# Kernel optimization log

Measured on AMD Instinct MI355X. Metric: run time of the kernel, lower is better.

Reference implementation:

```python
import jax, jax.numpy as jnp
import numpy as np

NUM_NODES = 50000
DIM = 64
NUM_LAYERS = 2
NUM_EDGES = 800000
EPS = 1e-12


def _l2_normalize(x):
    # F.normalize(x, dim=1): x / max(||x||_2, eps)
    n = jnp.sqrt(jnp.sum(x * x, axis=1, keepdims=True))
    return x / jnp.maximum(n, EPS)


def _lgconv(x, src, dst):
    # PyG LGConv: symmetric gcn_norm without self-loops.
    # deg computed at target nodes; out[dst] += d^-1/2[src] * d^-1/2[dst] * x[src]
    ones = jnp.ones(src.shape[0], dtype=x.dtype)
    deg = jax.ops.segment_sum(ones, dst, num_segments=NUM_NODES)
    dinv = jnp.where(deg > 0, 1.0 / jnp.sqrt(jnp.where(deg > 0, deg, 1.0)), 0.0)
    norm = dinv[src] * dinv[dst]  # [E]
    msg = norm[:, None] * x[src]  # [E, D] gather + scale
    return jax.ops.segment_sum(msg, dst, num_segments=NUM_NODES)


def _propagate(x, edge_index):
    src, dst = edge_index[0], edge_index[1]
    for _ in range(NUM_LAYERS):
        x = _lgconv(x, src, dst)
    return _l2_normalize(x)


def setup_inputs() -> dict:
    key = jax.random.key(0)
    k1, k2, k3, k4 = jax.random.split(key, 4)
    x = jax.random.normal(k1, (NUM_NODES, DIM), dtype=jnp.float32)
    alpha = jnp.ones((3,), dtype=jnp.float32)
    ei_t = jax.random.randint(k2, (2, NUM_EDGES), 0, NUM_NODES, dtype=jnp.int32)
    ei_y = jax.random.randint(k3, (2, NUM_EDGES), 0, NUM_NODES, dtype=jnp.int32)
    ei_c = jax.random.randint(k4, (2, NUM_EDGES), 0, NUM_NODES, dtype=jnp.int32)
    return {"x": x, "alpha": alpha, "edge_index_title": ei_t,
            "edge_index_year": ei_y, "edge_index_cat": ei_c}


def reference(x, alpha, edge_index_title, edge_index_year, edge_index_cat):
    x = _l2_normalize(x)
    x_title = _propagate(x, edge_index_title)
    x_year = _propagate(x, edge_index_year)
    x_cat = _propagate(x, edge_index_cat)
    w = jax.nn.softmax(alpha, axis=0)
    w = jnp.clip(w, 0.0001, None)
    w = w / jnp.sum(w)
    return w[0] * x_title + w[1] * x_year + w[2] * x_cat
```

## Files before the change

kernel.cpp:

```cpp
#include <hip/hip_runtime.h>
#include <hip/hip_bf16.h>

#define NUM_NODES 50000
#define DIM 64
#define NUM_EDGES 800000
#define NUM_GRAPHS 3
#define TOT_NODES (NUM_NODES * NUM_GRAPHS)
#define TOT_EDGES (NUM_EDGES * NUM_GRAPHS)
#define EPS 1e-12f

#define NB 196
#define TB (NB * NUM_GRAPHS)
#define P3_CHUNK 8192
#define P3_BLOCKS ((NUM_EDGES + P3_CHUNK - 1) / P3_CHUNK)
#define P4_CAP 6144

typedef unsigned short ushort_t;
typedef unsigned int uint_t;
typedef unsigned short ushort8v __attribute__((ext_vector_type(8)));

__device__ __forceinline__ float bf2f(ushort_t u) {
    return __uint_as_float(((uint_t)u) << 16);
}
__device__ __forceinline__ ushort_t f2bf(float f) {
    uint_t x = __float_as_uint(f);
    uint_t r = (x + 0x7FFFu + ((x >> 16) & 1u)) >> 16;
    return (ushort_t)r;
}

__global__ void l2norm_kernel(const float* __restrict__ in, ushort_t* __restrict__ out) {
    int row = blockIdx.x * (blockDim.x >> 6) + (threadIdx.x >> 6);
    int lane = threadIdx.x & 63;
    if (row >= NUM_NODES) return;
    float v = in[(long)row * DIM + lane];
    float s = v * v;
    #pragma unroll
    for (int off = 32; off > 0; off >>= 1)
        s += __shfl_xor(s, off, 64);
    float inv = 1.0f / fmaxf(sqrtf(s), EPS);
    out[(long)row * DIM + lane] = f2bf(v * inv);
}

__global__ void hist_coarse_kernel(const int* __restrict__ e0, const int* __restrict__ e1,
                                   const int* __restrict__ e2, int* __restrict__ bhist) {
    int g = blockIdx.y;
    const int* dst = ((g == 0) ? e0 : (g == 1) ? e1 : e2) + NUM_EDGES;
    __shared__ int h[NB];
    int t = threadIdx.x;
    for (int i = t; i < NB; i += 256) h[i] = 0;
    __syncthreads();
    int base = blockIdx.x * P3_CHUNK;
    int n = min(P3_CHUNK, NUM_EDGES - base);
    for (int i = t; i < n; i += 256)
        atomicAdd(&h[dst[base + i] >> 8], 1);
    __syncthreads();
    for (int i = t; i < NB; i += 256)
        if (h[i]) atomicAdd(&bhist[g * NB + i], h[i]);
}

__global__ void bucket_scan_kernel(const int* __restrict__ bhist, int* __restrict__ bbase,
                                   int* __restrict__ bcur) {
    int t = threadIdx.x;
    int v = (t < TB) ? bhist[t] : 0;
    __shared__ int sd[1024];
    sd[t] = v;
    __syncthreads();
    #pragma unroll
    for (int off = 1; off < 1024; off <<= 1) {
        int add = (t >= off) ? sd[t - off] : 0;
        __syncthreads();
        sd[t] += add;
        __syncthreads();
    }
    if (t < TB) {
        int ex = sd[t] - v;
        bbase[t] = ex;
        bcur[t] = ex;
    }
    if (t == 0) bbase[TB] = TOT_EDGES;
}

__global__ void partition_kernel(const int* __restrict__ e0, const int* __restrict__ e1,
                                 const int* __restrict__ e2,
                                 int* __restrict__ bcur, uint_t* __restrict__ part) {
    __shared__ uint_t recs[P3_CHUNK];
    __shared__ int h[NB], lstart[NB], gbase[NB], lcur[NB];
    __shared__ int sc[256];

    int g = blockIdx.y;
    const int* ei = (g == 0) ? e0 : (g == 1) ? e1 : e2;
    const int* srcp = ei;
    const int* dstp = ei + NUM_EDGES;
    int base = blockIdx.x * P3_CHUNK;
    int n = min(P3_CHUNK, NUM_EDGES - base);
    int t = threadIdx.x;

    for (int i = t; i < NB; i += 256) h[i] = 0;
    __syncthreads();
    for (int i = t; i < n; i += 256)
        atomicAdd(&h[dstp[base + i] >> 8], 1);
    __syncthreads();

    {
        int v = (t < NB) ? h[t] : 0;
        sc[t] = v;
        __syncthreads();
        #pragma unroll
        for (int off = 1; off < 256; off <<= 1) {
            int add = (t >= off) ? sc[t - off] : 0;
            __syncthreads();
            sc[t] += add;
            __syncthreads();
        }
        if (t < NB) {
            int ex = sc[t] - v;
            lstart[t] = ex;
            lcur[t] = ex;
            gbase[t] = (v > 0) ? atomicAdd(&bcur[g * NB + t], v) : 0;
        }
    }
    __syncthreads();

    for (int i = t; i < n; i += 256) {
        int s = srcp[base + i];
        int d = dstp[base + i];
        int pos = atomicAdd(&lcur[d >> 8], 1);
        recs[pos] = ((uint_t)d << 16) | (uint_t)s;
    }
    __syncthreads();

    for (int i = t; i < n; i += 256) {
        uint_t r = recs[i];
        int b = r >> 24;
        part[gbase[b] + (i - lstart[b])] = r;
    }
}

__global__ void bucket_sort_kernel(const uint_t* __restrict__ part, const int* __restrict__ bbase,
                                   ushort_t* __restrict__ esort, int* __restrict__ row_start,
                                   float* __restrict__ dinv) {
    __shared__ uint_t recs[P4_CAP];
    __shared__ int rstart[256], lcur[256];
    __shared__ int sc[256];

    int b = blockIdx.x;
    int g = b / NB;
    int bhi = b % NB;
    int s0 = bbase[b];
    int n = bbase[b + 1] - s0;
    int t = threadIdx.x;

    sc[t] = 0;
    __syncthreads();
    for (int i = t; i < n; i += 256) {
        uint_t r = part[s0 + i];
        recs[i] = r;
        atomicAdd(&sc[(r >> 16) & 255], 1);
    }
    __syncthreads();
    int v = sc[t];
    __syncthreads();
    sc[t] = v;
    __syncthreads();
    #pragma unroll
    for (int off = 1; off < 256; off <<= 1) {
        int add = (t >= off) ? sc[t - off] : 0;
        __syncthreads();
        sc[t] += add;
        __syncthreads();
    }
    int ex = sc[t] - v;
    rstart[t] = ex;
    lcur[t] = ex;

    int node = (bhi << 8) + t;
    if (node < NUM_NODES) {
        row_start[g * NUM_NODES + node] = s0 + ex;
        dinv[g * NUM_NODES + node] = (v > 0) ? rsqrtf((float)v) : 0.0f;
    }
    if (b == TB - 1 && t == 0) row_start[TOT_NODES] = TOT_EDGES;
    __syncthreads();

    for (int i = t; i < n; i += 256) {
        uint_t r = recs[i];
        int dl = (r >> 16) & 255;
        int pos = atomicAdd(&lcur[dl], 1);
        esort[s0 + pos] = (ushort_t)(r & 0xFFFFu);
    }
}

__global__ void conv1_all_kernel(const ushort_t* __restrict__ xn,
                                 const ushort_t* __restrict__ esort,
                                 const int* __restrict__ row_start,
                                 const float* __restrict__ dinv,
                                 ushort_t* __restrict__ bufA) {
    int row = blockIdx.x * (blockDim.x >> 6) + (threadIdx.x >> 6);
    int g = blockIdx.y;
    int lane = threadIdx.x & 63;
    int sub = lane >> 3;
    int li  = lane & 7;
    if (row >= NUM_NODES) return;

    int k = g * NUM_NODES + row;
    int start = __builtin_amdgcn_readfirstlane(row_start[k]);
    int end   = __builtin_amdgcn_readfirstlane(row_start[k + 1]);
    const float* dv = dinv + g * NUM_NODES;

    float a[8];
    #pragma unroll
    for (int j = 0; j < 8; ++j) a[j] = 0.0f;

    int i = start;
    for (; i + 16 <= end; i += 16) {
        int sA = esort[i + sub];
        int sB = esort[i + 8 + sub];
        float dA = dv[sA];
        float dB = dv[sB];
        ushort8v rA = *(const ushort8v*)(xn + (long)sA * DIM + li * 8);
        ushort8v rB = *(const ushort8v*)(xn + (long)sB * DIM + li * 8);
        #pragma unroll
        for (int j = 0; j < 8; ++j) a[j] += dA * bf2f(rA[j]);
        #pragma unroll
        for (int j = 0; j < 8; ++j) a[j] += dB * bf2f(rB[j]);
    }
    for (; i < end; i += 8) {
        int e = i + sub;
        if (e < end) {
            int s = esort[e];
            float d = dv[s];
            ushort8v r = *(const ushort8v*)(xn + (long)s * DIM + li * 8);
            #pragma unroll
            for (int j = 0; j < 8; ++j) a[j] += d * bf2f(r[j]);
        }
    }
    #pragma unroll
    for (int off = 8; off < 64; off <<= 1) {
        #pragma unroll
        for (int j = 0; j < 8; ++j)
            a[j] += __shfl_xor(a[j], off, 64);
    }
    float dt = dinv[k];
    float sc = dt * dt;
    if (sub == 0) {
        ushort8v o;
        #pragma unroll
        for (int j = 0; j < 8; ++j) o[j] = f2bf(a[j] * sc);
        *(ushort8v*)(bufA + (long)k * DIM + li * 8) = o;
    }
}

__global__ void conv2_finalize_kernel(const ushort_t* __restrict__ bufA,
                                      const ushort_t* __restrict__ esort,
                                      const int* __restrict__ row_start,
                                      const float* __restrict__ alpha,
                                      float* __restrict__ out) {
    int row = blockIdx.x * (blockDim.x >> 6) + (threadIdx.x >> 6);
    int lane = threadIdx.x & 63;
    int sub = lane >> 3;
    int li  = lane & 7;
    if (row >= NUM_NODES) return;

    float al0 = alpha[0], al1 = alpha[1], al2 = alpha[2];
    float m = fmaxf(al0, fmaxf(al1, al2));
    float e0 = expf(al0 - m), e1 = expf(al1 - m), e2 = expf(al2 - m);
    float es = e0 + e1 + e2;
    float w0 = fmaxf(e0 / es, 1e-4f);
    float w1 = fmaxf(e1 / es, 1e-4f);
    float w2 = fmaxf(e2 / es, 1e-4f);
    float ws = w0 + w1 + w2;

    float r[8];
    #pragma unroll
    for (int j = 0; j < 8; ++j) r[j] = 0.0f;

    #pragma unroll
    for (int g = 0; g < NUM_GRAPHS; ++g) {
        int k = g * NUM_NODES + row;
        int start = __builtin_amdgcn_readfirstlane(row_start[k]);
        int end   = __builtin_amdgcn_readfirstlane(row_start[k + 1]);
        const ushort_t* tbl = bufA + (long)g * NUM_NODES * DIM;

        float a[8];
        #pragma unroll
        for (int j = 0; j < 8; ++j) a[j] = 0.0f;

        int i = start;
        for (; i + 16 <= end; i += 16) {
            int sA = esort[i + sub];
            int sB = esort[i + 8 + sub];
            ushort8v rA = *(const ushort8v*)(tbl + (long)sA * DIM + li * 8);
            ushort8v rB = *(const ushort8v*)(tbl + (long)sB * DIM + li * 8);
            #pragma unroll
            for (int j = 0; j < 8; ++j) a[j] += bf2f(rA[j]);
            #pragma unroll
            for (int j = 0; j < 8; ++j) a[j] += bf2f(rB[j]);
        }
        for (; i < end; i += 8) {
            int e = i + sub;
            if (e < end) {
                int s = esort[e];
                ushort8v rr = *(const ushort8v*)(tbl + (long)s * DIM + li * 8);
                #pragma unroll
                for (int j = 0; j < 8; ++j) a[j] += bf2f(rr[j]);
            }
        }
        #pragma unroll
        for (int off = 8; off < 64; off <<= 1) {
            #pragma unroll
            for (int j = 0; j < 8; ++j)
                a[j] += __shfl_xor(a[j], off, 64);
        }
        float s = 0.0f;
        #pragma unroll
        for (int j = 0; j < 8; ++j) s += a[j] * a[j];
        #pragma unroll
        for (int off = 1; off < 8; off <<= 1)
            s += __shfl_xor(s, off, 64);
        float inv = 1.0f / fmaxf(sqrtf(s), EPS);
        float w = ((g == 0) ? w0 : (g == 1) ? w1 : w2) / ws * inv;
        #pragma unroll
        for (int j = 0; j < 8; ++j) r[j] += w * a[j];
    }

    if (sub == 0) {
        float4 o0 = make_float4(r[0], r[1], r[2], r[3]);
        float4 o1 = make_float4(r[4], r[5], r[6], r[7]);
        float* p = out + (long)row * DIM + li * 8;
        *(float4*)p = o0;
        *(float4*)(p + 4) = o1;
    }
}

extern "C" void kernel_launch(void* const* d_in, const int* in_sizes, int n_in,
                              void* d_out, int out_size, void* d_ws, size_t ws_size,
                              hipStream_t stream) {
    const float* x     = (const float*)d_in[0];
    const float* alpha = (const float*)d_in[1];
    const int* e0 = (const int*)d_in[2];
    const int* e1 = (const int*)d_in[3];
    const int* e2 = (const int*)d_in[4];
    float* out = (float*)d_out;

    ushort_t* xn   = (ushort_t*)d_ws;
    ushort_t* bufA = xn + (long)NUM_NODES * DIM;
    float* dinv    = (float*)(bufA + (long)TOT_NODES * DIM);
    int* row_start = (int*)(dinv + TOT_NODES);
    int* bhist     = row_start + 150016;
    int* bbase     = bhist + 640;
    int* bcur      = bbase + 640;
    uint_t* part   = (uint_t*)(bcur + 640);
    ushort_t* esort = (ushort_t*)(part + TOT_EDGES);

    const int wave_grid = (NUM_NODES * 64 + 255) / 256;

    l2norm_kernel<<<wave_grid, 256, 0, stream>>>(x, xn);

    hipMemsetAsync(bhist, 0, TB * sizeof(int), stream);
    {
        dim3 grd(P3_BLOCKS, NUM_GRAPHS);
        hist_coarse_kernel<<<grd, 256, 0, stream>>>(e0, e1, e2, bhist);
    }
    bucket_scan_kernel<<<1, 1024, 0, stream>>>(bhist, bbase, bcur);
    {
        dim3 grd(P3_BLOCKS, NUM_GRAPHS);
        partition_kernel<<<grd, 256, 0, stream>>>(e0, e1, e2, bcur, part);
    }
    bucket_sort_kernel<<<TB, 256, 0, stream>>>(part, bbase, esort, row_start, dinv);

    {
        dim3 grd(wave_grid, NUM_GRAPHS);
        conv1_all_kernel<<<grd, 256, 0, stream>>>(xn, esort, row_start, dinv, bufA);
    }
    conv2_finalize_kernel<<<wave_grid, 256, 0, stream>>>(bufA, esort, row_start, alpha, out);
}
```

Before: 255.8 us.

## Use fixed-capacity bucket slots, split conv2 per graph, add blend pass

Removes the coarse histogram and scan kernels by giving each destination bucket a fixed PCAP-sized slot in the partition buffer, with atomic counters giving offsets and row_end replacing row_start[k+1]. Conv2 is split into a per-graph kernel whose blocks interleave graphs for cache locality. It writes weighted normalized bf16 results, and a separate blend kernel sums the three graphs. Gathers now load uint4 words and unpack bf16 with shifts and masks. The cost is an extra bf16 round-trip for the outputs, and any bucket holding more than PCAP edges is silently truncated.

```diff
diff --git a/kernel.cpp b/kernel.cpp
--- a/kernel.cpp
+++ b/kernel.cpp
@@ -13,11 +13,12 @@
 #define TB (NB * NUM_GRAPHS)
 #define P3_CHUNK 8192
 #define P3_BLOCKS ((NUM_EDGES + P3_CHUNK - 1) / P3_CHUNK)
-#define P4_CAP 6144
+#define PCAP 5120
 
 typedef unsigned short ushort_t;
 typedef unsigned int uint_t;
 typedef unsigned short ushort8v __attribute__((ext_vector_type(8)));
+typedef unsigned int uint4v __attribute__((ext_vector_type(4)));
 
 __device__ __forceinline__ float bf2f(ushort_t u) {
     return __uint_as_float(((uint_t)u) << 16);
@@ -26,6 +27,27 @@
     uint_t x = __float_as_uint(f);
     uint_t r = (x + 0x7FFFu + ((x >> 16) & 1u)) >> 16;
     return (ushort_t)r;
+}
+
+__device__ __forceinline__ void unpack_fma(uint4v w, float d, float* a) {
+    a[0] += d * __uint_as_float(w[0] << 16);
+    a[1] += d * __uint_as_float(w[0] & 0xFFFF0000u);
+    a[2] += d * __uint_as_float(w[1] << 16);
+    a[3] += d * __uint_as_float(w[1] & 0xFFFF0000u);
+    a[4] += d * __uint_as_float(w[2] << 16);
+    a[5] += d * __uint_as_float(w[2] & 0xFFFF0000u);
+    a[6] += d * __uint_as_float(w[3] << 16);
+    a[7] += d * __uint_as_float(w[3] & 0xFFFF0000u);
+}
+__device__ __forceinline__ void unpack_add(uint4v w, float* a) {
+    a[0] += __uint_as_float(w[0] << 16);
+    a[1] += __uint_as_float(w[0] & 0xFFFF0000u);
+    a[2] += __uint_as_float(w[1] << 16);
+    a[3] += __uint_as_float(w[1] & 0xFFFF0000u);
+    a[4] += __uint_as_float(w[2] << 16);
+    a[5] += __uint_as_float(w[2] & 0xFFFF0000u);
+    a[6] += __uint_as_float(w[3] << 16);
+    a[7] += __uint_as_float(w[3] & 0xFFFF0000u);
 }
 
 __global__ void l2norm_kernel(const float* __restrict__ in, ushort_t* __restrict__ out) {
@@ -41,48 +63,9 @@
     out[(long)row * DIM + lane] = f2bf(v * inv);
 }
 
-__global__ void hist_coarse_kernel(const int* __restrict__ e0, const int* __restrict__ e1,
-                                   const int* __restrict__ e2, int* __restrict__ bhist) {
-    int g = blockIdx.y;
-    const int* dst = ((g == 0) ? e0 : (g == 1) ? e1 : e2) + NUM_EDGES;
-    __shared__ int h[NB];
-    int t = threadIdx.x;
-    for (int i = t; i < NB; i += 256) h[i] = 0;
-    __syncthreads();
-    int base = blockIdx.x * P3_CHUNK;
-    int n = min(P3_CHUNK, NUM_EDGES - base);
-    for (int i = t; i < n; i += 256)
-        atomicAdd(&h[dst[base + i] >> 8], 1);
-    __syncthreads();
-    for (int i = t; i < NB; i += 256)
-        if (h[i]) atomicAdd(&bhist[g * NB + i], h[i]);
-}
-
-__global__ void bucket_scan_kernel(const int* __restrict__ bhist, int* __restrict__ bbase,
-                                   int* __restrict__ bcur) {
-    int t = threadIdx.x;
-    int v = (t < TB) ? bhist[t] : 0;
-    __shared__ int sd[1024];
-    sd[t] = v;
-    __syncthreads();
-    #pragma unroll
-    for (int off = 1; off < 1024; off <<= 1) {
-        int add = (t >= off) ? sd[t - off] : 0;
-        __syncthreads();
-        sd[t] += add;
-        __syncthreads();
-    }
-    if (t < TB) {
-        int ex = sd[t] - v;
-        bbase[t] = ex;
-        bcur[t] = ex;
-    }
-    if (t == 0) bbase[TB] = TOT_EDGES;
-}
-
 __global__ void partition_kernel(const int* __restrict__ e0, const int* __restrict__ e1,
                                  const int* __restrict__ e2,
-                                 int* __restrict__ bcur, uint_t* __restrict__ part) {
+                                 int* __restrict__ gcnt, uint_t* __restrict__ part) {
     __shared__ uint_t recs[P3_CHUNK];
     __shared__ int h[NB], lstart[NB], gbase[NB], lcur[NB];
     __shared__ int sc[256];
@@ -116,7 +99,7 @@
             int ex = sc[t] - v;
             lstart[t] = ex;
             lcur[t] = ex;
-            gbase[t] = (v > 0) ? atomicAdd(&bcur[g * NB + t], v) : 0;
+            gbase[t] = (v > 0) ? atomicAdd(&gcnt[g * NB + t], v) : 0;
         }
     }
     __syncthreads();
@@ -132,22 +115,24 @@
     for (int i = t; i < n; i += 256) {
         uint_t r = recs[i];
         int b = r >> 24;
-        part[gbase[b] + (i - lstart[b])] = r;
-    }
-}
-
-__global__ void bucket_sort_kernel(const uint_t* __restrict__ part, const int* __restrict__ bbase,
+        int off = gbase[b] + (i - lstart[b]);
+        if (off < PCAP)
+            part[(long)(g * NB + b) * PCAP + off] = r;
+    }
+}
+
+__global__ void bucket_sort_kernel(const uint_t* __restrict__ part, const int* __restrict__ gcnt,
                                    ushort_t* __restrict__ esort, int* __restrict__ row_start,
-                                   float* __restrict__ dinv) {
-    __shared__ uint_t recs[P4_CAP];
-    __shared__ int rstart[256], lcur[256];
+                                   int* __restrict__ row_end, float* __restrict__ dinv) {
+    __shared__ uint_t recs[PCAP];
+    __shared__ int lcur[256];
     __shared__ int sc[256];
 
     int b = blockIdx.x;
     int g = b / NB;
     int bhi = b % NB;
-    int s0 = bbase[b];
-    int n = bbase[b + 1] - s0;
+    long s0 = (long)b * PCAP;
+    int n = min(gcnt[b], PCAP);
     int t = threadIdx.x;
 
     sc[t] = 0;
@@ -170,15 +155,15 @@
         __syncthreads();
     }
     int ex = sc[t] - v;
-    rstart[t] = ex;
     lcur[t] = ex;
 
     int node = (bhi << 8) + t;
     if (node < NUM_NODES) {
-        row_start[g * NUM_NODES + node] = s0 + ex;
-        dinv[g * NUM_NODES + node] = (v > 0) ? rsqrtf((float)v) : 0.0f;
-    }
-    if (b == TB - 1 && t == 0) row_start[TOT_NODES] = TOT_EDGES;
+        int k = g * NUM_NODES + node;
+        row_start[k] = (int)s0 + ex;
+        row_end[k]   = (int)s0 + ex + v;
+        dinv[k] = (v > 0) ? rsqrtf((float)v) : 0.0f;
+    }
     __syncthreads();
 
     for (int i = t; i < n; i += 256) {
@@ -192,6 +177,7 @@
 __global__ void conv1_all_kernel(const ushort_t* __restrict__ xn,
                                  const ushort_t* __restrict__ esort,
                                  const int* __restrict__ row_start,
+                                 const int* __restrict__ row_end,
                                  const float* __restrict__ dinv,
                                  ushort_t* __restrict__ bufA) {
     int row = blockIdx.x * (blockDim.x >> 6) + (threadIdx.x >> 6);
@@ -203,7 +189,7 @@
 
     int k = g * NUM_NODES + row;
     int start = __builtin_amdgcn_readfirstlane(row_start[k]);
-    int end   = __builtin_amdgcn_readfirstlane(row_start[k + 1]);
+    int end   = __builtin_amdgcn_readfirstlane(row_end[k]);
     const float* dv = dinv + g * NUM_NODES;
 
     float a[8];
@@ -216,21 +202,18 @@
         int sB = esort[i + 8 + sub];
         float dA = dv[sA];
         float dB = dv[sB];
-        ushort8v rA = *(const ushort8v*)(xn + (long)sA * DIM + li * 8);
-        ushort8v rB = *(const ushort8v*)(xn + (long)sB * DIM + li * 8);
-        #pragma unroll
-        for (int j = 0; j < 8; ++j) a[j] += dA * bf2f(rA[j]);
-        #pragma unroll
-        for (int j = 0; j < 8; ++j) a[j] += dB * bf2f(rB[j]);
+        uint4v rA = *(const uint4v*)(xn + (long)sA * DIM + li * 8);
+        uint4v rB = *(const uint4v*)(xn + (long)sB * DIM + li * 8);
+        unpack_fma(rA, dA, a);
+        unpack_fma(rB, dB, a);
     }
     for (; i < end; i += 8) {
         int e = i + sub;
         if (e < end) {
             int s = esort[e];
             float d = dv[s];
-            ushort8v r = *(const ushort8v*)(xn + (long)s * DIM + li * 8);
-            #pragma unroll
-            for (int j = 0; j < 8; ++j) a[j] += d * bf2f(r[j]);
+            uint4v r = *(const uint4v*)(xn + (long)s * DIM + li * 8);
+            unpack_fma(r, d, a);
         }
     }
     #pragma unroll
@@ -240,25 +223,40 @@
             a[j] += __shfl_xor(a[j], off, 64);
     }
     float dt = dinv[k];
-    float sc = dt * dt;
+    float scl = dt * dt;
     if (sub == 0) {
         ushort8v o;
         #pragma unroll
-        for (int j = 0; j < 8; ++j) o[j] = f2bf(a[j] * sc);
+        for (int j = 0; j < 8; ++j) o[j] = f2bf(a[j] * scl);
         *(ushort8v*)(bufA + (long)k * DIM + li * 8) = o;
     }
 }
 
-__global__ void conv2_finalize_kernel(const ushort_t* __restrict__ bufA,
-                                      const ushort_t* __restrict__ esort,
-                                      const int* __restrict__ row_start,
-                                      const float* __restrict__ alpha,
-                                      float* __restrict__ out) {
-    int row = blockIdx.x * (blockDim.x >> 6) + (threadIdx.x >> 6);
+__global__ void conv2_kernel(const ushort_t* __restrict__ bufA,
+                             const ushort_t* __restrict__ esort,
+                             const int* __restrict__ row_start,
+                             const int* __restrict__ row_end,
+                             const float* __restrict__ alpha,
+                             ushort_t* __restrict__ ybuf) {
+    const int gmap[8]   = {0, 1, 2, 0, 1, 2, 0, 1};
+    const int idxmap[8] = {0, 0, 0, 1, 1, 1, 2, 2};
+    const int cntmap[8] = {3, 3, 2, 3, 3, 2, 3, 3};
+
+    int x = blockIdx.x & 7;
+    int j = blockIdx.x >> 3;
+    int g = gmap[x];
+    int idx = idxmap[x];
+    int cnt = cntmap[x];
+    int chunk = (NUM_NODES + cnt - 1) / cnt;
+
+    int row_local = j * 4 + (threadIdx.x >> 6);
+    if (row_local >= chunk) return;
+    int row = idx * chunk + row_local;
+    if (row >= NUM_NODES) return;
+
     int lane = threadIdx.x & 63;
     int sub = lane >> 3;
     int li  = lane & 7;
-    if (row >= NUM_NODES) return;
 
     float al0 = alpha[0], al1 = alpha[1], al2 = alpha[2];
     float m = fmaxf(al0, fmaxf(al1, al2));
@@ -268,67 +266,71 @@
     float w1 = fmaxf(e1 / es, 1e-4f);
     float w2 = fmaxf(e2 / es, 1e-4f);
     float ws = w0 + w1 + w2;
-
+    float w = ((g == 0) ? w0 : (g == 1) ? w1 : w2) / ws;
+
+    int k = g * NUM_NODES + row;
+    int start = __builtin_amdgcn_readfirstlane(row_start[k]);
+    int end   = __builtin_amdgcn_readfirstlane(row_end[k]);
+    const ushort_t* tbl = bufA + (long)g * NUM_NODES * DIM;
+
+    float a[8];
+    #pragma unroll
+    for (int jj = 0; jj < 8; ++jj) a[jj] = 0.0f;
+
+    int i = start;
+    for (; i + 16 <= end; i += 16) {
+        int sA = esort[i + sub];
+        int sB = esort[i + 8 + sub];
+        uint4v rA = *(const uint4v*)(tbl + (long)sA * DIM + li * 8);
+        uint4v rB = *(const uint4v*)(tbl + (long)sB * DIM + li * 8);
+        unpack_add(rA, a);
+        unpack_add(rB, a);
+    }
+    for (; i < end; i += 8) {
+        int e = i + sub;
+        if (e < end) {
+            int s = esort[e];
+            uint4v r = *(const uint4v*)(tbl + (long)s * DIM + li * 8);
+            unpack_add(r, a);
+        }
+    }
+    #pragma unroll
+    for (int off = 8; off < 64; off <<= 1) {
+        #pragma unroll
+        for (int jj = 0; jj < 8; ++jj)
+            a[jj] += __shfl_xor(a[jj], off, 64);
+    }
+    float s = 0.0f;
+    #pragma unroll
+    for (int jj = 0; jj < 8; ++jj) s += a[jj] * a[jj];
+    #pragma unroll
+    for (int off = 1; off < 8; off <<= 1)
+        s += __shfl_xor(s, off, 64);
+    float scl = w / fmaxf(sqrtf(s), EPS);
+
+    if (sub == 0) {
+        ushort8v o;
+        #pragma unroll
+        for (int jj = 0; jj < 8; ++jj) o[jj] = f2bf(a[jj] * scl);
+        *(ushort8v*)(ybuf + (long)k * DIM + li * 8) = o;
+    }
+}
+
+__global__ void blend_kernel(const ushort_t* __restrict__ ybuf, float* __restrict__ out) {
+    int i = blockIdx.x * blockDim.x + threadIdx.x;
+    if (i >= NUM_NODES * DIM / 8) return;
+    uint4v w0 = *(const uint4v*)(ybuf + (long)i * 8);
+    uint4v w1 = *(const uint4v*)(ybuf + (long)NUM_NODES * DIM + (long)i * 8);
+    uint4v w2 = *(const uint4v*)(ybuf + 2L * NUM_NODES * DIM + (long)i * 8);
     float r[8];
     #pragma unroll
-    for (int j = 0; j < 8; ++j) r[j] = 0.0f;
-
-    #pragma unroll
-    for (int g = 0; g < NUM_GRAPHS; ++g) {
-        int k = g * NUM_NODES + row;
-        int start = __builtin_amdgcn_readfirstlane(row_start[k]);
-        int end   = __builtin_amdgcn_readfirstlane(row_start[k + 1]);
-        const ushort_t* tbl = bufA + (long)g * NUM_NODES * DIM;
-
-        float a[8];
-        #pragma unroll
-        for (int j = 0; j < 8; ++j) a[j] = 0.0f;
-
-        int i = start;
-        for (; i + 16 <= end; i += 16) {
-            int sA = esort[i + sub];
-            int sB = esort[i + 8 + sub];
-            ushort8v rA = *(const ushort8v*)(tbl + (long)sA * DIM + li * 8);
-            ushort8v rB = *(const ushort8v*)(tbl + (long)sB * DIM + li * 8);
-            #pragma unroll
-            for (int j = 0; j < 8; ++j) a[j] += bf2f(rA[j]);
-            #pragma unroll
-            for (int j = 0; j < 8; ++j) a[j] += bf2f(rB[j]);
-        }
-        for (; i < end; i += 8) {
-            int e = i + sub;
-            if (e < end) {
-                int s = esort[e];
-                ushort8v rr = *(const ushort8v*)(tbl + (long)s * DIM + li * 8);
-                #pragma unroll
-                for (int j = 0; j < 8; ++j) a[j] += bf2f(rr[j]);
-            }
-        }
-        #pragma unroll
-        for (int off = 8; off < 64; off <<= 1) {
-            #pragma unroll
-            for (int j = 0; j < 8; ++j)
-                a[j] += __shfl_xor(a[j], off, 64);
-        }
-        float s = 0.0f;
-        #pragma unroll
-        for (int j = 0; j < 8; ++j) s += a[j] * a[j];
-        #pragma unroll
-        for (int off = 1; off < 8; off <<= 1)
-            s += __shfl_xor(s, off, 64);
-        float inv = 1.0f / fmaxf(sqrtf(s), EPS);
-        float w = ((g == 0) ? w0 : (g == 1) ? w1 : w2) / ws * inv;
-        #pragma unroll
-        for (int j = 0; j < 8; ++j) r[j] += w * a[j];
-    }
-
-    if (sub == 0) {
-        float4 o0 = make_float4(r[0], r[1], r[2], r[3]);
-        float4 o1 = make_float4(r[4], r[5], r[6], r[7]);
-        float* p = out + (long)row * DIM + li * 8;
-        *(float4*)p = o0;
-        *(float4*)(p + 4) = o1;
-    }
+    for (int jj = 0; jj < 8; ++jj) r[jj] = 0.0f;
+    unpack_add(w0, r);
+    unpack_add(w1, r);
+    unpack_add(w2, r);
+    float* p = out + (long)i * 8;
+    *(float4*)p = make_float4(r[0], r[1], r[2], r[3]);
+    *(float4*)(p + 4) = make_float4(r[4], r[5], r[6], r[7]);
 }
 
 extern "C" void kernel_launch(void* const* d_in, const int* in_sizes, int n_in,
@@ -343,33 +345,35 @@
 
     ushort_t* xn   = (ushort_t*)d_ws;
     ushort_t* bufA = xn + (long)NUM_NODES * DIM;
-    float* dinv    = (float*)(bufA + (long)TOT_NODES * DIM);
+    ushort_t* ybuf = bufA + (long)TOT_NODES * DIM;
+    float* dinv    = (float*)(ybuf + (long)TOT_NODES * DIM);
     int* row_start = (int*)(dinv + TOT_NODES);
-    int* bhist     = row_start + 150016;
-    int* bbase     = bhist + 640;
-    int* bcur      = bbase + 640;
-    uint_t* part   = (uint_t*)(bcur + 640);
-    ushort_t* esort = (ushort_t*)(part + TOT_EDGES);
+    int* row_end   = row_start + 150016;
+    int* gcnt      = row_end + 150016;
+    uint_t* part   = (uint_t*)(gcnt + 640);
+    ushort_t* esort = (ushort_t*)(part + (long)TB * PCAP);
 
     const int wave_grid = (NUM_NODES * 64 + 255) / 256;
 
     l2norm_kernel<<<wave_grid, 256, 0, stream>>>(x, xn);
 
-    hipMemsetAsync(bhist, 0, TB * sizeof(int), stream);
+    hipMemsetAsync(gcnt, 0, TB * sizeof(int), stream);
     {
         dim3 grd(P3_BLOCKS, NUM_GRAPHS);
-        hist_coarse_kernel<<<grd, 256, 0, stream>>>(e0, e1, e2, bhist);
-    }
-    bucket_scan_kernel<<<1, 1024, 0, stream>>>(bhist, bbase, bcur);
-    {
-        dim3 grd(P3_BLOCKS, NUM_GRAPHS);
-        partition_kernel<<<grd, 256, 0, stream>>>(e0, e1, e2, bcur, part);
-    }
-    bucket_sort_kernel<<<TB, 256, 0, stream>>>(part, bbase, esort, row_start, dinv);
+        partition_kernel<<<grd, 256, 0, stream>>>(e0, e1, e2, gcnt, part);
+    }
+    bucket_sort_kernel<<<TB, 256, 0, stream>>>(part, gcnt, esort, row_start, row_end, dinv);
 
     {
         dim3 grd(wave_grid, NUM_GRAPHS);
-        conv1_all_kernel<<<grd, 256, 0, stream>>>(xn, esort, row_start, dinv, bufA);
-    }
-    conv2_finalize_kernel<<<wave_grid, 256, 0, stream>>>(bufA, esort, row_start, alpha, out);
-}
+        conv1_all_kernel<<<grd, 256, 0, stream>>>(xn, esort, row_start, row_end, dinv, bufA);
+    }
+    {
+        int blocks = 8 * ((25000 + 3) / 4);
+        conv2_kernel<<<blocks, 256, 0, stream>>>(bufA, esort, row_start, row_end, alpha, ybuf);
+    }
+    {
+        int n8 = NUM_NODES * DIM / 8;
+        blend_kernel<<<(n8 + 255) / 256, 256, 0, stream>>>(ybuf, out);
+    }
+}
```

After: 293.0 us. 1.15x slower.
